# Kernel tuning notes

Measured on AMD Instinct MI355X. Metric: run time of the kernel, lower is better.

The kernel has to match this reference:

```python
import jax, jax.numpy as jnp
import numpy as np

N_NODES = 100000
N_EDGES = 3200000
IN_FEAT = 512
HIDDEN = 16
N_CLASSES = 40


def gcn_conv(x, W, b, row, col, n):
    """PyG-style GCNConv: linear transform, add self-loops, symmetric deg^-1/2
    normalization, gather-scatter aggregation, bias."""
    self_idx = jnp.arange(n, dtype=row.dtype)
    row_sl = jnp.concatenate([row, self_idx])  # [E + N]
    col_sl = jnp.concatenate([col, self_idx])
    deg = jax.ops.segment_sum(jnp.ones_like(row_sl, dtype=x.dtype), row_sl, num_segments=n)
    dinv = jnp.where(deg > 0, jax.lax.rsqrt(deg), 0.0)
    norm = dinv[row_sl] * dinv[col_sl]  # [E + N]
    h = x @ W  # [n, out] -- transform first (cheap since out dim is small)
    msg = h[col_sl] * norm[:, None]  # gather + scale
    out = jax.ops.segment_sum(msg, row_sl, num_segments=n)  # scatter-add
    return out + b


def setup_inputs() -> dict:
    key = jax.random.key(0)
    k1, k2, k3, k4, k5 = jax.random.split(key, 5)
    x = jax.random.normal(k1, (N_NODES, IN_FEAT), dtype=jnp.float32)
    edge_index = jax.random.randint(k2, (2, N_EDGES), 0, N_NODES, dtype=jnp.int64)
    # Glorot-style init for linear weights
    W1 = jax.random.normal(k3, (IN_FEAT, HIDDEN), dtype=jnp.float32) / np.sqrt(IN_FEAT)
    b1 = jnp.zeros((HIDDEN,), dtype=jnp.float32)
    W2 = jax.random.normal(k4, (HIDDEN, N_CLASSES), dtype=jnp.float32) / np.sqrt(HIDDEN)
    b2 = jnp.zeros((N_CLASSES,), dtype=jnp.float32)
    return {"x": x, "edge_index": edge_index, "W1": W1, "b1": b1, "W2": W2, "b2": b2}


def reference(x, edge_index, W1, b1, W2, b2):
    row, col = edge_index[0], edge_index[1]
    n = x.shape[0]
    h = jax.nn.relu(gcn_conv(x, W1, b1, row, col, n))
    # dropout is identity at inference (training=False)
    out = gcn_conv(h, W2, b2, row, col, n)
    return jax.nn.log_softmax(out, axis=1)
```

## Files before the change

kernel.cpp:

```cpp
#include <hip/hip_runtime.h>

#define NFEAT 512
#define HID 16
#define NCLS 40
#define BROWS 256
#define BCAP 16384

typedef unsigned int uint32;
typedef float f4 __attribute__((ext_vector_type(4)));

__device__ __forceinline__ uint32 f2bf(float f) {
    uint32 u = __float_as_uint(f);
    return (u + 0x7FFFu + ((u >> 16) & 1u)) >> 16;
}
__device__ __forceinline__ float bf2f(uint32 h) {
    return __uint_as_float(h << 16);
}

__global__ void k_zero(int* __restrict__ p, int m) {
    int i = blockIdx.x * blockDim.x + threadIdx.x;
    if (i < m) p[i] = 0;
}

__global__ __launch_bounds__(256) void k_pairs(const int* __restrict__ row,
                                               const int* __restrict__ col,
                                               int* __restrict__ bcur,
                                               uint32* __restrict__ pairs, int E, int nb) {
    __shared__ int lhist[512];
    __shared__ int lbase[512];
    const int E4 = E >> 2;
    const int chunk4 = (E4 + gridDim.x - 1) / gridDim.x;
    const int s4 = blockIdx.x * chunk4;
    const int e4 = min(s4 + chunk4, E4);
    const int4* rp = reinterpret_cast<const int4*>(row);
    const int4* cp = reinterpret_cast<const int4*>(col);

    for (int b = threadIdx.x; b < nb; b += 256) lhist[b] = 0;
    __syncthreads();
    for (int i4 = s4 + (int)threadIdx.x; i4 < e4; i4 += 256) {
        int4 r4 = rp[i4];
        atomicAdd(&lhist[r4.x >> 8], 1);
        atomicAdd(&lhist[r4.y >> 8], 1);
        atomicAdd(&lhist[r4.z >> 8], 1);
        atomicAdd(&lhist[r4.w >> 8], 1);
    }
    if (blockIdx.x == gridDim.x - 1) {
        for (int i = E4 * 4 + (int)threadIdx.x; i < E; i += 256)
            atomicAdd(&lhist[row[i] >> 8], 1);
    }
    __syncthreads();
    for (int b = threadIdx.x; b < nb; b += 256) {
        int h = lhist[b];
        lbase[b] = h ? atomicAdd(&bcur[b], h) : 0;
        lhist[b] = 0;
    }
    __syncthreads();
    for (int i4 = s4 + (int)threadIdx.x; i4 < e4; i4 += 256) {
        int4 r4 = rp[i4];
        int4 c4 = cp[i4];
#pragma unroll
        for (int u = 0; u < 4; u++) {
            int r = (&r4.x)[u], c = (&c4.x)[u];
            int b = r >> 8;
            int off = lbase[b] + atomicAdd(&lhist[b], 1);
            if (off < BCAP)
                pairs[(size_t)b * BCAP + off] = ((uint32)(r & 255) << 17) | (uint32)c;
        }
    }
    if (blockIdx.x == gridDim.x - 1) {
        for (int i = E4 * 4 + (int)threadIdx.x; i < E; i += 256) {
            int r = row[i], c = col[i];
            int b = r >> 8;
            int off = lbase[b] + atomicAdd(&lhist[b], 1);
            if (off < BCAP)
                pairs[(size_t)b * BCAP + off] = ((uint32)(r & 255) << 17) | (uint32)c;
        }
    }
}

__global__ __launch_bounds__(256) void k_deg(const int* __restrict__ bcur,
                                             const uint32* __restrict__ pairs,
                                             int* __restrict__ cnt,
                                             float* __restrict__ dinv, int n) {
    __shared__ int lh[BROWS];
    int b = blockIdx.x;
    int bo = b * BCAP;
    int c2 = min(bcur[b], BCAP);
    lh[threadIdx.x] = 0;
    __syncthreads();
    for (int p = bo + (int)threadIdx.x; p < bo + c2; p += 256)
        atomicAdd(&lh[pairs[p] >> 17], 1);
    __syncthreads();
    int i = b * BROWS + threadIdx.x;
    if (i < n) {
        int c = lh[threadIdx.x];
        cnt[i] = c;
        dinv[i] = rsqrtf((float)c + 1.0f);
    }
}

__global__ __launch_bounds__(256, 4) void k_fused(const int* __restrict__ bcur,
                                                  const uint32* __restrict__ pairs,
                                                  const int* __restrict__ cnt,
                                                  int* __restrict__ csr,
                                                  int* __restrict__ start,
                                                  int* __restrict__ end,
                                                  const float* __restrict__ x,
                                                  const float* __restrict__ W,
                                                  const float* __restrict__ dinv,
                                                  uint32* __restrict__ g1,
                                                  int n, int nbCsr) {
    __shared__ float smem[8704];
    const int tid = threadIdx.x;

    if (blockIdx.x < (uint32)nbCsr) {
        int* sm   = (int*)smem;
        int* lcur = (int*)smem + 256;
        int b = blockIdx.x;
        int base = b * BROWS;
        int i = base + tid;
        int bo = b * BCAP;
        int cntb = min(bcur[b], BCAP);
        int e2 = bo + cntb;

        int c = (i < n) ? cnt[i] : 0;
        sm[tid] = c;
        __syncthreads();
        for (int off = 1; off < 256; off <<= 1) {
            int t = (tid >= off) ? sm[tid - off] : 0;
            __syncthreads();
            sm[tid] += t;
            __syncthreads();
        }
        int excl = sm[tid] - c;
        lcur[tid] = excl;
        if (i < n) {
            start[i] = bo + excl;
            end[i]   = bo + excl + c;
        }
        __syncthreads();
        for (int p = bo + tid; p < e2; p += 256) {
            uint32 pk = pairs[p];
            int off = atomicAdd(&lcur[pk >> 17], 1);
            csr[bo + off] = (int)(pk & 0x1FFFFu);
        }
        return;
    }

    float* Wl = smem;
    const int ks = tid & 7;
    const int g  = tid >> 3;

#pragma unroll
    for (int i = 0; i < 8; i++) {
        int fidx = tid + i * 256;
        int k = fidx >> 2, j4 = fidx & 3;
        float4 v = reinterpret_cast<const float4*>(W)[fidx];
        *reinterpret_cast<float4*>(&Wl[k * 16 + (k >> 2) * 4 + j4 * 4]) = v;
    }
    __syncthreads();

    const int rbase = (blockIdx.x - nbCsr) * 64 + g * 2;
    const int r0 = min(rbase, n - 1);
    const int r1 = min(rbase + 1, n - 1);
    const f4* xq0 = reinterpret_cast<const f4*>(x + (size_t)r0 * NFEAT);
    const f4* xq1 = reinterpret_cast<const f4*>(x + (size_t)r1 * NFEAT);

    float acc[2][16];
#pragma unroll
    for (int rr = 0; rr < 2; rr++)
#pragma unroll
        for (int j = 0; j < 16; j++) acc[rr][j] = 0.f;

    f4 xv[2], xn1[2], xn2[2];
    xv[0]  = __builtin_nontemporal_load(&xq0[ks]);
    xv[1]  = __builtin_nontemporal_load(&xq1[ks]);
    xn1[0] = __builtin_nontemporal_load(&xq0[8 + ks]);
    xn1[1] = __builtin_nontemporal_load(&xq1[8 + ks]);

    for (int c = 0; c < 16; c++) {
        if (c < 14) {
            xn2[0] = __builtin_nontemporal_load(&xq0[(c + 2) * 8 + ks]);
            xn2[1] = __builtin_nontemporal_load(&xq1[(c + 2) * 8 + ks]);
        }
#pragma unroll
        for (int m = 0; m < 4; m++) {
            int k = c * 32 + ks * 4 + m;
            const float* wrow = &Wl[k * 16 + (k >> 2) * 4];
            float4 wv[4];
#pragma unroll
            for (int j4 = 0; j4 < 4; j4++)
                wv[j4] = *reinterpret_cast<const float4*>(wrow + j4 * 4);
#pragma unroll
            for (int rr = 0; rr < 2; rr++) {
                float xs = xv[rr][m];
#pragma unroll
                for (int j4 = 0; j4 < 4; j4++) {
                    acc[rr][j4 * 4 + 0] = fmaf(xs, wv[j4].x, acc[rr][j4 * 4 + 0]);
                    acc[rr][j4 * 4 + 1] = fmaf(xs, wv[j4].y, acc[rr][j4 * 4 + 1]);
                    acc[rr][j4 * 4 + 2] = fmaf(xs, wv[j4].z, acc[rr][j4 * 4 + 2]);
                    acc[rr][j4 * 4 + 3] = fmaf(xs, wv[j4].w, acc[rr][j4 * 4 + 3]);
                }
            }
        }
        xv[0] = xn1[0];
        xv[1] = xn1[1];
        xn1[0] = xn2[0];
        xn1[1] = xn2[1];
    }

#pragma unroll
    for (int off = 1; off < 8; off <<= 1)
#pragma unroll
        for (int rr = 0; rr < 2; rr++)
#pragma unroll
            for (int j = 0; j < 16; j++)
                acc[rr][j] += __shfl_xor(acc[rr][j], off, 8);

    if (ks == 0) {
#pragma unroll
        for (int rr = 0; rr < 2; rr++) {
            int r = rbase + rr;
            if (r < n) {
                float dr = dinv[r];
                uint32 us[8];
#pragma unroll
                for (int q = 0; q < 8; q++) {
                    uint32 lo = f2bf(dr * acc[rr][q * 2]);
                    uint32 hi = f2bf(dr * acc[rr][q * 2 + 1]);
                    us[q] = lo | (hi << 16);
                }
                uint4* o = reinterpret_cast<uint4*>(g1 + (size_t)r * 8);
                o[0] = make_uint4(us[0], us[1], us[2], us[3]);
                o[1] = make_uint4(us[4], us[5], us[6], us[7]);
            }
        }
    }
}

__global__ __launch_bounds__(256) void k_agg1(const uint32* __restrict__ g1,
                                              const int* __restrict__ start,
                                              const int* __restrict__ end,
                                              const int* __restrict__ csr,
                                              const float* __restrict__ dinv,
                                              const float* __restrict__ b1,
                                              uint32* __restrict__ g2, int n) {
    int g = threadIdx.x >> 3;
    int l = threadIdx.x & 7;
    int r = blockIdx.x * 32 + g;
    if (r >= n) return;
    int s = start[r], e = end[r];
    float a0 = 0.f, a1 = 0.f;
    int p = s;
    for (; p + 16 <= e; p += 16) {
        int c[16];
#pragma unroll
        for (int u = 0; u < 16; u++) c[u] = csr[p + u];
        uint32 hv[16];
#pragma unroll
        for (int u = 0; u < 16; u++) hv[u] = g1[c[u] * 8 + l];
#pragma unroll
        for (int u = 0; u < 16; u++) {
            a0 += bf2f(hv[u] & 0xFFFFu);
            a1 += bf2f(hv[u] >> 16);
        }
    }
    for (; p + 8 <= e; p += 8) {
        int c[8];
#pragma unroll
        for (int u = 0; u < 8; u++) c[u] = csr[p + u];
        uint32 hv[8];
#pragma unroll
        for (int u = 0; u < 8; u++) hv[u] = g1[c[u] * 8 + l];
#pragma unroll
        for (int u = 0; u < 8; u++) {
            a0 += bf2f(hv[u] & 0xFFFFu);
            a1 += bf2f(hv[u] >> 16);
        }
    }
    for (; p < e; p++) {
        uint32 h = g1[csr[p] * 8 + l];
        a0 += bf2f(h & 0xFFFFu);
        a1 += bf2f(h >> 16);
    }
    uint32 hs = g1[r * 8 + l];
    float dr = dinv[r];
    float z0 = fmaf(dr, a0 + bf2f(hs & 0xFFFFu), b1[2 * l]);
    float z1 = fmaf(dr, a1 + bf2f(hs >> 16), b1[2 * l + 1]);
    g2[r * 8 + l] = f2bf(dr * fmaxf(z0, 0.f)) | (f2bf(dr * fmaxf(z1, 0.f)) << 16);
}

__global__ __launch_bounds__(256) void k_agg2(const uint32* __restrict__ g2,
                                              const int* __restrict__ start,
                                              const int* __restrict__ end,
                                              const int* __restrict__ csr,
                                              const float* __restrict__ dinv,
                                              const float* __restrict__ W2,
                                              const float* __restrict__ b2,
                                              float* __restrict__ out, int n) {
    __shared__ float vsm[32][17];
    int g = threadIdx.x >> 3;
    int l = threadIdx.x & 7;
    int r = blockIdx.x * 32 + g;
    float a0 = 0.f, a1 = 0.f;
    if (r < n) {
        int s = start[r], e = end[r];
        int p = s;
        for (; p + 16 <= e; p += 16) {
            int c[16];
#pragma unroll
            for (int u = 0; u < 16; u++) c[u] = csr[p + u];
            uint32 hv[16];
#pragma unroll
            for (int u = 0; u < 16; u++) hv[u] = g2[c[u] * 8 + l];
#pragma unroll
            for (int u = 0; u < 16; u++) {
                a0 += bf2f(hv[u] & 0xFFFFu);
                a1 += bf2f(hv[u] >> 16);
            }
        }
        for (; p + 8 <= e; p += 8) {
            int c[8];
#pragma unroll
            for (int u = 0; u < 8; u++) c[u] = csr[p + u];
            uint32 hv[8];
#pragma unroll
            for (int u = 0; u < 8; u++) hv[u] = g2[c[u] * 8 + l];
#pragma unroll
            for (int u = 0; u < 8; u++) {
                a0 += bf2f(hv[u] & 0xFFFFu);
                a1 += bf2f(hv[u] >> 16);
            }
        }
        for (; p < e; p++) {
            uint32 h = g2[csr[p] * 8 + l];
            a0 += bf2f(h & 0xFFFFu);
            a1 += bf2f(h >> 16);
        }
        uint32 hs = g2[r * 8 + l];
        float dr = dinv[r];
        a0 = dr * (a0 + bf2f(hs & 0xFFFFu));
        a1 = dr * (a1 + bf2f(hs >> 16));
    }
    vsm[g][2 * l] = a0;
    vsm[g][2 * l + 1] = a1;
    __syncthreads();
    if (r >= n) return;

    float vloc[16];
#pragma unroll
    for (int k = 0; k < 16; k++) vloc[k] = vsm[g][k];

    float z[5];
#pragma unroll
    for (int i = 0; i < 5; i++) z[i] = b2[l + 8 * i];
#pragma unroll
    for (int k = 0; k < 16; k++) {
        float vk = vloc[k];
        const float* wk = W2 + k * NCLS;
#pragma unroll
        for (int i = 0; i < 5; i++) z[i] = fmaf(vk, wk[l + 8 * i], z[i]);
    }
    float m = z[0];
#pragma unroll
    for (int i = 1; i < 5; i++) m = fmaxf(m, z[i]);
#pragma unroll
    for (int off = 1; off < 8; off <<= 1) m = fmaxf(m, __shfl_xor(m, off, 8));
    float ssum = 0.f;
#pragma unroll
    for (int i = 0; i < 5; i++) ssum += __expf(z[i] - m);
#pragma unroll
    for (int off = 1; off < 8; off <<= 1) ssum += __shfl_xor(ssum, off, 8);
    float ls = m + logf(ssum);
    float* o = out + (size_t)r * NCLS;
#pragma unroll
    for (int i = 0; i < 5; i++) o[l + 8 * i] = z[i] - ls;
}


extern "C" void kernel_launch(void* const* d_in, const int* in_sizes, int n_in,
                              void* d_out, int out_size, void* d_ws, size_t ws_size,
                              hipStream_t stream) {
    const float* x  = (const float*)d_in[0];
    const int*   ei = (const int*)d_in[1];
    const float* W1 = (const float*)d_in[2];
    const float* b1 = (const float*)d_in[3];
    const float* W2 = (const float*)d_in[4];
    const float* b2 = (const float*)d_in[5];

    const int n = in_sizes[0] / NFEAT;
    const int E = in_sizes[1] / 2;
    const int* row = ei;
    const int* col = ei + E;
    const int nb = (n + BROWS - 1) / BROWS;

    char* w = (char*)d_ws;
    auto alloc = [&](size_t bytes) {
        void* p = (void*)w;
        w += (bytes + 255) & ~(size_t)255;
        return p;
    };
    int*    start = (int*)alloc((size_t)n * 4);
    int*    end   = (int*)alloc((size_t)n * 4);
    int*    cnt   = (int*)alloc((size_t)n * 4);
    int*    bcur  = (int*)alloc(2048);
    float*  dinv  = (float*)alloc((size_t)n * 4);
    int*    csr   = (int*)alloc((size_t)nb * BCAP * 4);
    uint32* pairs = (uint32*)alloc((size_t)nb * BCAP * 4);
    uint32* g1    = (uint32*)alloc((size_t)n * HID * 2);
    uint32* g2    = (uint32*)alloc((size_t)n * HID * 2);

    k_zero<<<1, 512, 0, stream>>>(bcur, nb);
    k_pairs<<<512, 256, 0, stream>>>(row, col, bcur, pairs, E, nb);
    k_deg<<<nb, 256, 0, stream>>>(bcur, pairs, cnt, dinv, n);
    k_fused<<<nb + (n + 63) / 64, 256, 0, stream>>>(bcur, pairs, cnt, csr, start, end,
                                                    x, W1, dinv, g1, n, nb);
    k_agg1<<<(n + 31) / 32, 256, 0, stream>>>(g1, start, end, csr, dinv, b1, g2, n);
    k_agg2<<<(n + 31) / 32, 256, 0, stream>>>(g2, start, end, csr, dinv, W2, b2,
                                              (float*)d_out, n);
}
```

Before: 176.1 us.

## Store W1 as bf16 in LDS, one row per group, raise occupancy

The GEMM part of the fused kernel now keeps W1 in shared memory as packed bf16 pairs, which halves LDS use. Each 8-thread group handles one row instead of two, so accumulator registers drop and launch bounds can rise from 4 to 8 blocks per CU. k_pairs also gets twice as many blocks. The aim is more resident waves to hide the latency of streaming x, at the cost of bf16 rounding of the weights and half the reuse of each LDS weight read across rows.

```diff
diff --git a/kernel.cpp b/kernel.cpp
--- a/kernel.cpp
+++ b/kernel.cpp
@@ -99,7 +99,7 @@
     }
 }
 
-__global__ __launch_bounds__(256, 4) void k_fused(const int* __restrict__ bcur,
+__global__ __launch_bounds__(256, 8) void k_fused(const int* __restrict__ bcur,
                                                   const uint32* __restrict__ pairs,
                                                   const int* __restrict__ cnt,
                                                   int* __restrict__ csr,
@@ -110,7 +110,7 @@
                                                   const float* __restrict__ dinv,
                                                   uint32* __restrict__ g1,
                                                   int n, int nbCsr) {
-    __shared__ float smem[8704];
+    __shared__ uint32 smem[4352];
     const int tid = threadIdx.x;
 
     if (blockIdx.x < (uint32)nbCsr) {
@@ -147,94 +147,71 @@
         return;
     }
 
-    float* Wl = smem;
+#pragma unroll
+    for (int i = 0; i < 16; i++) {
+        int idx = tid + i * 256;
+        int k = idx >> 3, p = idx & 7;
+        const float* wp = W + k * 16 + p * 2;
+        uint32 lo = f2bf(wp[0]);
+        uint32 hi = f2bf(wp[1]);
+        smem[k * 8 + (k >> 2) * 2 + p] = lo | (hi << 16);
+    }
+    __syncthreads();
+
     const int ks = tid & 7;
     const int g  = tid >> 3;
-
-#pragma unroll
-    for (int i = 0; i < 8; i++) {
-        int fidx = tid + i * 256;
-        int k = fidx >> 2, j4 = fidx & 3;
-        float4 v = reinterpret_cast<const float4*>(W)[fidx];
-        *reinterpret_cast<float4*>(&Wl[k * 16 + (k >> 2) * 4 + j4 * 4]) = v;
-    }
-    __syncthreads();
-
-    const int rbase = (blockIdx.x - nbCsr) * 64 + g * 2;
-    const int r0 = min(rbase, n - 1);
-    const int r1 = min(rbase + 1, n - 1);
-    const f4* xq0 = reinterpret_cast<const f4*>(x + (size_t)r0 * NFEAT);
-    const f4* xq1 = reinterpret_cast<const f4*>(x + (size_t)r1 * NFEAT);
-
-    float acc[2][16];
-#pragma unroll
-    for (int rr = 0; rr < 2; rr++)
-#pragma unroll
-        for (int j = 0; j < 16; j++) acc[rr][j] = 0.f;
-
-    f4 xv[2], xn1[2], xn2[2];
-    xv[0]  = __builtin_nontemporal_load(&xq0[ks]);
-    xv[1]  = __builtin_nontemporal_load(&xq1[ks]);
-    xn1[0] = __builtin_nontemporal_load(&xq0[8 + ks]);
-    xn1[1] = __builtin_nontemporal_load(&xq1[8 + ks]);
+    const int r = (blockIdx.x - nbCsr) * 32 + g;
+    const f4* xq = reinterpret_cast<const f4*>(x + (size_t)min(r, n - 1) * NFEAT);
+
+    float acc[16];
+#pragma unroll
+    for (int j = 0; j < 16; j++) acc[j] = 0.f;
+
+    f4 xv, xn1, xn2;
+    xv  = __builtin_nontemporal_load(&xq[ks]);
+    xn1 = __builtin_nontemporal_load(&xq[8 + ks]);
 
     for (int c = 0; c < 16; c++) {
-        if (c < 14) {
-            xn2[0] = __builtin_nontemporal_load(&xq0[(c + 2) * 8 + ks]);
-            xn2[1] = __builtin_nontemporal_load(&xq1[(c + 2) * 8 + ks]);
-        }
+        if (c < 14)
+            xn2 = __builtin_nontemporal_load(&xq[(c + 2) * 8 + ks]);
 #pragma unroll
         for (int m = 0; m < 4; m++) {
             int k = c * 32 + ks * 4 + m;
-            const float* wrow = &Wl[k * 16 + (k >> 2) * 4];
-            float4 wv[4];
-#pragma unroll
-            for (int j4 = 0; j4 < 4; j4++)
-                wv[j4] = *reinterpret_cast<const float4*>(wrow + j4 * 4);
-#pragma unroll
-            for (int rr = 0; rr < 2; rr++) {
-                float xs = xv[rr][m];
-#pragma unroll
-                for (int j4 = 0; j4 < 4; j4++) {
-                    acc[rr][j4 * 4 + 0] = fmaf(xs, wv[j4].x, acc[rr][j4 * 4 + 0]);
-                    acc[rr][j4 * 4 + 1] = fmaf(xs, wv[j4].y, acc[rr][j4 * 4 + 1]);
-                    acc[rr][j4 * 4 + 2] = fmaf(xs, wv[j4].z, acc[rr][j4 * 4 + 2]);
-                    acc[rr][j4 * 4 + 3] = fmaf(xs, wv[j4].w, acc[rr][j4 * 4 + 3]);
-                }
+            const uint32* wrow = &smem[k * 8 + (k >> 2) * 2];
+            uint32 w8[8];
+            *reinterpret_cast<uint4*>(&w8[0]) = *reinterpret_cast<const uint4*>(wrow);
+            *reinterpret_cast<uint4*>(&w8[4]) = *reinterpret_cast<const uint4*>(wrow + 4);
+            float xs = xv[m];
+#pragma unroll
+            for (int p = 0; p < 8; p++) {
+                float w0 = __uint_as_float(w8[p] << 16);
+                float w1 = __uint_as_float(w8[p] & 0xFFFF0000u);
+                acc[2 * p]     = fmaf(xs, w0, acc[2 * p]);
+                acc[2 * p + 1] = fmaf(xs, w1, acc[2 * p + 1]);
             }
         }
-        xv[0] = xn1[0];
-        xv[1] = xn1[1];
-        xn1[0] = xn2[0];
-        xn1[1] = xn2[1];
+        xv = xn1;
+        xn1 = xn2;
     }
 
 #pragma unroll
     for (int off = 1; off < 8; off <<= 1)
 #pragma unroll
-        for (int rr = 0; rr < 2; rr++)
-#pragma unroll
-            for (int j = 0; j < 16; j++)
-                acc[rr][j] += __shfl_xor(acc[rr][j], off, 8);
-
-    if (ks == 0) {
-#pragma unroll
-        for (int rr = 0; rr < 2; rr++) {
-            int r = rbase + rr;
-            if (r < n) {
-                float dr = dinv[r];
-                uint32 us[8];
-#pragma unroll
-                for (int q = 0; q < 8; q++) {
-                    uint32 lo = f2bf(dr * acc[rr][q * 2]);
-                    uint32 hi = f2bf(dr * acc[rr][q * 2 + 1]);
-                    us[q] = lo | (hi << 16);
-                }
-                uint4* o = reinterpret_cast<uint4*>(g1 + (size_t)r * 8);
-                o[0] = make_uint4(us[0], us[1], us[2], us[3]);
-                o[1] = make_uint4(us[4], us[5], us[6], us[7]);
-            }
-        }
+        for (int j = 0; j < 16; j++)
+            acc[j] += __shfl_xor(acc[j], off, 8);
+
+    if (ks == 0 && r < n) {
+        float dr = dinv[r];
+        uint32 us[8];
+#pragma unroll
+        for (int q = 0; q < 8; q++) {
+            uint32 lo = f2bf(dr * acc[q * 2]);
+            uint32 hi = f2bf(dr * acc[q * 2 + 1]);
+            us[q] = lo | (hi << 16);
+        }
+        uint4* o = reinterpret_cast<uint4*>(g1 + (size_t)r * 8);
+        o[0] = make_uint4(us[0], us[1], us[2], us[3]);
+        o[1] = make_uint4(us[4], us[5], us[6], us[7]);
     }
 }
 
@@ -393,6 +370,7 @@
     const int* row = ei;
     const int* col = ei + E;
     const int nb = (n + BROWS - 1) / BROWS;
+    const int ngemm = (n + 31) / 32;
 
     char* w = (char*)d_ws;
     auto alloc = [&](size_t bytes) {
@@ -411,10 +389,10 @@
     uint32* g2    = (uint32*)alloc((size_t)n * HID * 2);
 
     k_zero<<<1, 512, 0, stream>>>(bcur, nb);
-    k_pairs<<<512, 256, 0, stream>>>(row, col, bcur, pairs, E, nb);
+    k_pairs<<<1024, 256, 0, stream>>>(row, col, bcur, pairs, E, nb);
     k_deg<<<nb, 256, 0, stream>>>(bcur, pairs, cnt, dinv, n);
-    k_fused<<<nb + (n + 63) / 64, 256, 0, stream>>>(bcur, pairs, cnt, csr, start, end,
-                                                    x, W1, dinv, g1, n, nb);
+    k_fused<<<nb + ngemm, 256, 0, stream>>>(bcur, pairs, cnt, csr, start, end,
+                                            x, W1, dinv, g1, n, nb);
     k_agg1<<<(n + 31) / 32, 256, 0, stream>>>(g1, start, end, csr, dinv, b1, g2, n);
     k_agg2<<<(n + 31) / 32, 256, 0, stream>>>(g2, start, end, csr, dinv, W2, b2,
                                               (float*)d_out, n);
```

New measurement: 322.7 us. +83.2%, slower.
